# Kernel tuning notes

Measured on AMD Instinct MI355X. Metric: run time of the kernel, lower is better.

The kernel has to match this reference:

```python
import jax, jax.numpy as jnp
import numpy as np

B, T, F, H = 8192, 256, 64, 50

def setup_inputs() -> dict:
    key = jax.random.key(0)
    ks = jax.random.split(key, 6)
    s = 0.1
    x = jax.random.normal(ks[0], (B, T, F), dtype=jnp.float32)
    W = jax.random.normal(ks[1], (F, 3 * H), dtype=jnp.float32) * s   # input kernel [z|r|h]
    U = jax.random.normal(ks[2], (H, 3 * H), dtype=jnp.float32) * s   # recurrent kernel
    b = jax.random.normal(ks[3], (2, 3 * H), dtype=jnp.float32) * s   # [input bias; recurrent bias] (reset_after=True)
    Wd = jax.random.normal(ks[4], (H, 1), dtype=jnp.float32) * s
    bd = jax.random.normal(ks[5], (1,), dtype=jnp.float32) * s
    return {"x": x, "W": W, "U": U, "b": b, "Wd": Wd, "bd": bd}

def _gru_last_hidden(x, W, U, b):
    # Precompute input projections for all timesteps: [B,T,3H]
    xp = jnp.einsum('btf,fg->btg', x, W) + b[0]
    xp = jnp.transpose(xp, (1, 0, 2))  # [T,B,3H] for scan over time
    bi = b[1]

    def step(h, xt):
        rp = h @ U + bi                       # recurrent projection [B,3H]
        xz, xr, xh = jnp.split(xt, 3, axis=-1)
        rz, rr, rh = jnp.split(rp, 3, axis=-1)
        z = jax.nn.sigmoid(xz + rz)
        r = jax.nn.sigmoid(xr + rr)
        hh = jnp.tanh(xh + r * rh)            # reset_after=True formulation
        h_new = z * h + (1.0 - z) * hh
        return h_new, None

    h0 = jnp.zeros((x.shape[0], U.shape[0]), dtype=x.dtype)
    h_last, _ = jax.lax.scan(step, h0, xp)
    return h_last

def reference(x, W, U, b, Wd, bd):
    h = _gru_last_hidden(x, W, U, b)   # [B,H]
    # Dropout is identity at inference time
    return h @ Wd + bd                 # [B,1]
```

## Files before the change

### kernel.cpp

```cpp
#include <hip/hip_runtime.h>
#include <hip/hip_bf16.h>


typedef __attribute__((ext_vector_type(8))) short s16x8;
typedef __attribute__((ext_vector_type(4))) float f32x4;

#define TS 256

__device__ __forceinline__ unsigned short f2bf(float f) {
  unsigned int v = __builtin_bit_cast(unsigned int, f);
  v += 0x7FFFu + ((v >> 16) & 1u);
  return (unsigned short)(v >> 16);
}
__device__ __forceinline__ unsigned int cvtpk(float a, float b) {
  unsigned int r;
  asm("v_cvt_pk_bf16_f32 %0, %1, %2" : "=v"(r) : "v"(a), "v"(b));
  return r;
}
__device__ __forceinline__ float rcpf(float a) {
  return __builtin_amdgcn_rcpf(a);
}

#define RAWBAR()                                                \
  do {                                                          \
    asm volatile("s_waitcnt lgkmcnt(0)" ::: "memory");          \
    __builtin_amdgcn_sched_barrier(0);                          \
    __builtin_amdgcn_s_barrier();                               \
  } while (0)

__global__ __launch_bounds__(256, 2) void gru_fused(
    const float* __restrict__ x,  const float* __restrict__ W,
    const float* __restrict__ U,  const float* __restrict__ b,
    const float* __restrict__ Wd, const float* __restrict__ bdp,
    float* __restrict__ out)
{
  __shared__ __align__(16) unsigned short xbuf[2][2][512];
  __shared__ __align__(16) unsigned short hbuf[2][2][512];
  __shared__ float red[4][16];

  const int tid = threadIdx.x;
  const int l   = tid & 63;
  const int w   = tid >> 6;
  const int lhi = l >> 4, llo = l & 15;
  const int row0 = blockIdx.x << 4;
  const int u = (w << 4) + llo;

  ((unsigned long long*)hbuf)[tid] = 0ULL;

  const float sZR = -1.44269504088896f;
  const float sH  =  2.88539008177793f;
  float bzS = 0.f, brS = 0.f, bh0S = 0.f, bh1S = 0.f;
  if (u < 50) {
    bzS  = sZR * (b[u]      + b[150 + u]);
    brS  = sZR * (b[50 + u] + b[200 + u]);
    bh0S = sH * b[100 + u];
    bh1S = sH * b[250 + u];
  }

  s16x8 breg[3][4];
  #pragma unroll
  for (int g = 0; g < 3; ++g) {
    const float sc = (g < 2) ? sZR : sH;
    #pragma unroll
    for (int kc = 0; kc < 4; ++kc) {
      s16x8 f;
      #pragma unroll
      for (int i = 0; i < 8; ++i) {
        const int k = kc * 32 + lhi * 8 + i;
        float v = 0.f;
        if (u < 50 && k < 114)
          v = (k < 64) ? W[k * 150 + g * 50 + u]
                       : U[(k - 64) * 150 + g * 50 + u];
        f[i] = (short)f2bf(v * sc);
      }
      breg[g][kc] = f;
    }
  }

  const int sc    = tid >> 7;
  const int sla   = (tid >> 1) & 63;
  const int shalf = tid & 1;
  const float* xp = x + (long)(row0 + (sla & 15)) * (TS * 64)
                      + sc * 32 + (sla >> 4) * 8 + shalf * 4;
  unsigned long long* const xd0 =
      (unsigned long long*)&xbuf[0][sc][sla * 8 + shalf * 4];
  unsigned long long* const xd1 =
      (unsigned long long*)&xbuf[1][sc][sla * 8 + shalf * 4];

  unsigned short* const hst =
      &hbuf[0][u >> 5][(((u & 31) >> 3) * 16 + lhi * 4) * 8 + (u & 7)];

  {
    const f32x4 t0 = *(const f32x4*)xp;
    *xd0 = ((unsigned long long)cvtpk(t0[2], t0[3]) << 32) | cvtpk(t0[0], t0[1]);
    const f32x4 t1 = *(const f32x4*)(xp + 64);
    *xd1 = ((unsigned long long)cvtpk(t1[2], t1[3]) << 32) | cvtpk(t1[0], t1[1]);
  }
  f32x4 X0, X1, X2, X3, X4, X5, X6, X7;
  X2 = *(const f32x4*)(xp + 2 * 64);
  X3 = *(const f32x4*)(xp + 3 * 64);
  X4 = *(const f32x4*)(xp + 4 * 64);
  X5 = *(const f32x4*)(xp + 5 * 64);
  __syncthreads();

  f32x4 LA0 = {bzS, bzS, bzS, bzS}, LA1 = {brS, brS, brS, brS},
        LA2 = {bh0S, bh0S, bh0S, bh0S}, LB0, LB1, LB2;
  {
    const s16x8 a0 = *(const s16x8*)&xbuf[0][0][l * 8];
    const s16x8 a1 = *(const s16x8*)&xbuf[0][1][l * 8];
    LA0 = __builtin_amdgcn_mfma_f32_16x16x32_bf16(a0, breg[0][0], LA0, 0,0,0);
    LA0 = __builtin_amdgcn_mfma_f32_16x16x32_bf16(a1, breg[0][1], LA0, 0,0,0);
    LA1 = __builtin_amdgcn_mfma_f32_16x16x32_bf16(a0, breg[1][0], LA1, 0,0,0);
    LA1 = __builtin_amdgcn_mfma_f32_16x16x32_bf16(a1, breg[1][1], LA1, 0,0,0);
    LA2 = __builtin_amdgcn_mfma_f32_16x16x32_bf16(a0, breg[2][0], LA2, 0,0,0);
    LA2 = __builtin_amdgcn_mfma_f32_16x16x32_bf16(a1, breg[2][1], LA2, 0,0,0);
  }
  __syncthreads();

  float h0 = 0.f, h1 = 0.f, h2 = 0.f, h3 = 0.f;

#define STEP(T, XC, XL, C0, C1, C2, N0, N1, N2)                                \
  {                                                                            \
    const int tl = ((T) + 6 > TS - 1) ? (TS - 1) : ((T) + 6);                  \
    XL = *(const f32x4*)(xp + (long)tl * 64);                                  \
    const int PAR = (T) & 1;                                                   \
    const s16x8 a2 = *(const s16x8*)&hbuf[PAR][0][l * 8];                      \
    const s16x8 a3 = *(const s16x8*)&hbuf[PAR][1][l * 8];                      \
    f32x4 g0 = {0.f, 0.f, 0.f, 0.f}, g1 = {0.f, 0.f, 0.f, 0.f};               \
    f32x4 g2 = {bh1S, bh1S, bh1S, bh1S};                                       \
    g0 = __builtin_amdgcn_mfma_f32_16x16x32_bf16(a2, breg[0][2], g0, 0,0,0);   \
    g0 = __builtin_amdgcn_mfma_f32_16x16x32_bf16(a3, breg[0][3], g0, 0,0,0);   \
    g1 = __builtin_amdgcn_mfma_f32_16x16x32_bf16(a2, breg[1][2], g1, 0,0,0);   \
    g1 = __builtin_amdgcn_mfma_f32_16x16x32_bf16(a3, breg[1][3], g1, 0,0,0);   \
    g2 = __builtin_amdgcn_mfma_f32_16x16x32_bf16(a2, breg[2][2], g2, 0,0,0);   \
    g2 = __builtin_amdgcn_mfma_f32_16x16x32_bf16(a3, breg[2][3], g2, 0,0,0);   \
    const s16x8 a0 = *(const s16x8*)&xbuf[PAR ^ 1][0][l * 8];                  \
    const s16x8 a1 = *(const s16x8*)&xbuf[PAR ^ 1][1][l * 8];                  \
    N0 = (f32x4){bzS, bzS, bzS, bzS};                                          \
    N1 = (f32x4){brS, brS, brS, brS};                                          \
    N2 = (f32x4){bh0S, bh0S, bh0S, bh0S};                                      \
    N0 = __builtin_amdgcn_mfma_f32_16x16x32_bf16(a0, breg[0][0], N0, 0,0,0);   \
    N0 = __builtin_amdgcn_mfma_f32_16x16x32_bf16(a1, breg[0][1], N0, 0,0,0);   \
    N1 = __builtin_amdgcn_mfma_f32_16x16x32_bf16(a0, breg[1][0], N1, 0,0,0);   \
    N1 = __builtin_amdgcn_mfma_f32_16x16x32_bf16(a1, breg[1][1], N1, 0,0,0);   \
    N2 = __builtin_amdgcn_mfma_f32_16x16x32_bf16(a0, breg[2][0], N2, 0,0,0);   \
    N2 = __builtin_amdgcn_mfma_f32_16x16x32_bf16(a1, breg[2][1], N2, 0,0,0);   \
    *(PAR ? xd1 : xd0) =                                                       \
        ((unsigned long long)cvtpk(XC[2], XC[3]) << 32) | cvtpk(XC[0], XC[1]); \
    _Pragma("unroll")                                                          \
    for (int r = 0; r < 4; ++r) {                                              \
      float hv = (r == 0) ? h0 : (r == 1) ? h1 : (r == 2) ? h2 : h3;           \
      const float z  = rcpf(1.f + exp2f(C0[r] + g0[r]));                       \
      const float rr = rcpf(1.f + exp2f(C1[r] + g1[r]));                       \
      const float q  = rcpf(1.f + exp2f(fmaf(rr, g2[r], C2[r])));              \
      const float hh = fmaf(-2.f, q, 1.f);                                     \
      hv = fmaf(z, hv - hh, hh);                                               \
      if (r == 0) h0 = hv; else if (r == 1) h1 = hv;                           \
      else if (r == 2) h2 = hv; else h3 = hv;                                  \
      hst[(PAR ^ 1) * 1024 + r * 8] = (unsigned short)cvtpk(hv, 0.f);          \
    }                                                                          \
    RAWBAR();                                                                  \
  }

  for (int t = 0; t < TS; t += 8) {
    STEP(t + 0, X2, X6, LA0, LA1, LA2, LB0, LB1, LB2)
    STEP(t + 1, X3, X7, LB0, LB1, LB2, LA0, LA1, LA2)
    STEP(t + 2, X4, X0, LA0, LA1, LA2, LB0, LB1, LB2)
    STEP(t + 3, X5, X1, LB0, LB1, LB2, LA0, LA1, LA2)
    STEP(t + 4, X6, X2, LA0, LA1, LA2, LB0, LB1, LB2)
    STEP(t + 5, X7, X3, LB0, LB1, LB2, LA0, LA1, LA2)
    STEP(t + 6, X0, X4, LA0, LA1, LA2, LB0, LB1, LB2)
    STEP(t + 7, X1, X5, LB0, LB1, LB2, LA0, LA1, LA2)
  }
#undef STEP

  const float Wdv = (u < 50) ? Wd[u] : 0.f;
  float p0 = h0 * Wdv, p1 = h1 * Wdv, p2 = h2 * Wdv, p3 = h3 * Wdv;
  #pragma unroll
  for (int m = 1; m < 16; m <<= 1) {
    p0 += __shfl_xor(p0, m);
    p1 += __shfl_xor(p1, m);
    p2 += __shfl_xor(p2, m);
    p3 += __shfl_xor(p3, m);
  }
  if (llo == 0) {
    red[w][lhi * 4 + 0] = p0;
    red[w][lhi * 4 + 1] = p1;
    red[w][lhi * 4 + 2] = p2;
    red[w][lhi * 4 + 3] = p3;
  }
  __syncthreads();
  if (tid < 16)
    out[row0 + tid] =
        red[0][tid] + red[1][tid] + red[2][tid] + red[3][tid] + bdp[0];
}

extern "C" void kernel_launch(void* const* d_in, const int* in_sizes, int n_in,
                              void* d_out, int out_size, void* d_ws, size_t ws_size,
                              hipStream_t stream) {
  const float* x   = (const float*)d_in[0];
  const float* W   = (const float*)d_in[1];
  const float* U   = (const float*)d_in[2];
  const float* b   = (const float*)d_in[3];
  const float* Wd  = (const float*)d_in[4];
  const float* bdp = (const float*)d_in[5];
  float* out = (float*)d_out;
  gru_fused<<<dim3(512), dim3(256), 0, stream>>>(x, W, U, b, Wd, bdp, out);
}
```

Measured before the change: 798.1 us.

## Halve rows per block, double grid and occupancy, simplify x pipeline

Each block now handles 8 batch rows instead of 16, and the grid doubles to 1024 blocks. Launch bounds rise to 4 blocks per SM so more independent recurrences can interleave and hide the serial per-step latency. The input projection is no longer software-pipelined one step ahead. It is computed inside the same step, alongside the recurrent MFMAs, with a shallower register prefetch of x. Half of each 16-row MFMA tile is now wasted on zero padding, and only lanes holding real rows run the gate math. That doubles the total MFMA work.

Result: slower. 887.2 us (+11.2%).

```diff
diff --git a/kernel.cpp b/kernel.cpp
--- a/kernel.cpp
+++ b/kernel.cpp
@@ -1,8 +1,8 @@
 #include <hip/hip_runtime.h>
-#include <hip/hip_bf16.h>
 
 
 typedef __attribute__((ext_vector_type(8))) short s16x8;
+typedef __attribute__((ext_vector_type(2))) float f32x2;
 typedef __attribute__((ext_vector_type(4))) float f32x4;
 
 #define TS 256
@@ -28,7 +28,7 @@
     __builtin_amdgcn_s_barrier();                               \
   } while (0)
 
-__global__ __launch_bounds__(256, 2) void gru_fused(
+__global__ __launch_bounds__(256, 4) void gru_fused(
     const float* __restrict__ x,  const float* __restrict__ W,
     const float* __restrict__ U,  const float* __restrict__ b,
     const float* __restrict__ Wd, const float* __restrict__ bdp,
@@ -36,16 +36,19 @@
 {
   __shared__ __align__(16) unsigned short xbuf[2][2][512];
   __shared__ __align__(16) unsigned short hbuf[2][2][512];
-  __shared__ float red[4][16];
+  __shared__ float red[4][8];
 
   const int tid = threadIdx.x;
   const int l   = tid & 63;
   const int w   = tid >> 6;
   const int lhi = l >> 4, llo = l & 15;
-  const int row0 = blockIdx.x << 4;
+  const int row0 = blockIdx.x << 3;
   const int u = (w << 4) + llo;
 
-  ((unsigned long long*)hbuf)[tid] = 0ULL;
+  ((unsigned long long*)xbuf)[tid]       = 0ULL;
+  ((unsigned long long*)xbuf)[tid + 256] = 0ULL;
+  ((unsigned long long*)hbuf)[tid]       = 0ULL;
+  ((unsigned long long*)hbuf)[tid + 256] = 0ULL;
 
   const float sZR = -1.44269504088896f;
   const float sH  =  2.88539008177793f;
@@ -60,7 +63,7 @@
   s16x8 breg[3][4];
   #pragma unroll
   for (int g = 0; g < 3; ++g) {
-    const float sc = (g < 2) ? sZR : sH;
+    const float scg = (g < 2) ? sZR : sH;
     #pragma unroll
     for (int kc = 0; kc < 4; ++kc) {
       s16x8 f;
@@ -71,106 +74,86 @@
         if (u < 50 && k < 114)
           v = (k < 64) ? W[k * 150 + g * 50 + u]
                        : U[(k - 64) * 150 + g * 50 + u];
-        f[i] = (short)f2bf(v * sc);
+        f[i] = (short)f2bf(v * scg);
       }
       breg[g][kc] = f;
     }
   }
 
-  const int sc    = tid >> 7;
-  const int sla   = (tid >> 1) & 63;
-  const int shalf = tid & 1;
-  const float* xp = x + (long)(row0 + (sla & 15)) * (TS * 64)
-                      + sc * 32 + (sla >> 4) * 8 + shalf * 4;
-  unsigned long long* const xd0 =
-      (unsigned long long*)&xbuf[0][sc][sla * 8 + shalf * 4];
-  unsigned long long* const xd1 =
-      (unsigned long long*)&xbuf[1][sc][sla * 8 + shalf * 4];
+  const int sc   = tid >> 7;
+  const int rem  = tid & 127;
+  const int srow = rem >> 4;
+  const int koff = (rem & 15) << 1;
+  const float* xp = x + (long)(row0 + srow) * (TS * 64) + sc * 32 + koff;
+  const int sidx = ((((koff >> 3) * 16 + srow) << 3) + (koff & 7)) >> 1;
+  unsigned int* const xd0 = (unsigned int*)&xbuf[0][sc][0] + sidx;
+  unsigned int* const xd1 = (unsigned int*)&xbuf[1][sc][0] + sidx;
 
   unsigned short* const hst =
-      &hbuf[0][u >> 5][(((u & 31) >> 3) * 16 + lhi * 4) * 8 + (u & 7)];
+      &hbuf[0][u >> 5][((((u & 31) >> 3) * 16 + lhi * 4) << 3) + (u & 7)];
 
   {
-    const f32x4 t0 = *(const f32x4*)xp;
-    *xd0 = ((unsigned long long)cvtpk(t0[2], t0[3]) << 32) | cvtpk(t0[0], t0[1]);
-    const f32x4 t1 = *(const f32x4*)(xp + 64);
-    *xd1 = ((unsigned long long)cvtpk(t1[2], t1[3]) << 32) | cvtpk(t1[0], t1[1]);
+    const f32x2 t0 = *(const f32x2*)xp;
+    *xd0 = cvtpk(t0[0], t0[1]);
   }
-  f32x4 X0, X1, X2, X3, X4, X5, X6, X7;
-  X2 = *(const f32x4*)(xp + 2 * 64);
-  X3 = *(const f32x4*)(xp + 3 * 64);
-  X4 = *(const f32x4*)(xp + 4 * 64);
-  X5 = *(const f32x4*)(xp + 5 * 64);
-  __syncthreads();
-
-  f32x4 LA0 = {bzS, bzS, bzS, bzS}, LA1 = {brS, brS, brS, brS},
-        LA2 = {bh0S, bh0S, bh0S, bh0S}, LB0, LB1, LB2;
-  {
-    const s16x8 a0 = *(const s16x8*)&xbuf[0][0][l * 8];
-    const s16x8 a1 = *(const s16x8*)&xbuf[0][1][l * 8];
-    LA0 = __builtin_amdgcn_mfma_f32_16x16x32_bf16(a0, breg[0][0], LA0, 0,0,0);
-    LA0 = __builtin_amdgcn_mfma_f32_16x16x32_bf16(a1, breg[0][1], LA0, 0,0,0);
-    LA1 = __builtin_amdgcn_mfma_f32_16x16x32_bf16(a0, breg[1][0], LA1, 0,0,0);
-    LA1 = __builtin_amdgcn_mfma_f32_16x16x32_bf16(a1, breg[1][1], LA1, 0,0,0);
-    LA2 = __builtin_amdgcn_mfma_f32_16x16x32_bf16(a0, breg[2][0], LA2, 0,0,0);
-    LA2 = __builtin_amdgcn_mfma_f32_16x16x32_bf16(a1, breg[2][1], LA2, 0,0,0);
-  }
+  f32x2 R0 = *(const f32x2*)(xp + 1 * 64);
+  f32x2 R1 = *(const f32x2*)(xp + 2 * 64);
+  f32x2 R2 = *(const f32x2*)(xp + 3 * 64);
+  f32x2 R3 = *(const f32x2*)(xp + 4 * 64);
   __syncthreads();
 
   float h0 = 0.f, h1 = 0.f, h2 = 0.f, h3 = 0.f;
 
-#define STEP(T, XC, XL, C0, C1, C2, N0, N1, N2)                                \
+#define STEP(T, CUR)                                                           \
   {                                                                            \
-    const int tl = ((T) + 6 > TS - 1) ? (TS - 1) : ((T) + 6);                  \
-    XL = *(const f32x4*)(xp + (long)tl * 64);                                  \
     const int PAR = (T) & 1;                                                   \
+    const s16x8 a0 = *(const s16x8*)&xbuf[PAR][0][l * 8];                      \
+    const s16x8 a1 = *(const s16x8*)&xbuf[PAR][1][l * 8];                      \
     const s16x8 a2 = *(const s16x8*)&hbuf[PAR][0][l * 8];                      \
     const s16x8 a3 = *(const s16x8*)&hbuf[PAR][1][l * 8];                      \
-    f32x4 g0 = {0.f, 0.f, 0.f, 0.f}, g1 = {0.f, 0.f, 0.f, 0.f};               \
-    f32x4 g2 = {bh1S, bh1S, bh1S, bh1S};                                       \
+    f32x4 g0 = {bzS, bzS, bzS, bzS};                                           \
+    g0 = __builtin_amdgcn_mfma_f32_16x16x32_bf16(a0, breg[0][0], g0, 0,0,0);   \
+    g0 = __builtin_amdgcn_mfma_f32_16x16x32_bf16(a1, breg[0][1], g0, 0,0,0);   \
     g0 = __builtin_amdgcn_mfma_f32_16x16x32_bf16(a2, breg[0][2], g0, 0,0,0);   \
     g0 = __builtin_amdgcn_mfma_f32_16x16x32_bf16(a3, breg[0][3], g0, 0,0,0);   \
+    f32x4 g1 = {brS, brS, brS, brS};                                           \
+    g1 = __builtin_amdgcn_mfma_f32_16x16x32_bf16(a0, breg[1][0], g1, 0,0,0);   \
+    g1 = __builtin_amdgcn_mfma_f32_16x16x32_bf16(a1, breg[1][1], g1, 0,0,0);   \
     g1 = __builtin_amdgcn_mfma_f32_16x16x32_bf16(a2, breg[1][2], g1, 0,0,0);   \
     g1 = __builtin_amdgcn_mfma_f32_16x16x32_bf16(a3, breg[1][3], g1, 0,0,0);   \
-    g2 = __builtin_amdgcn_mfma_f32_16x16x32_bf16(a2, breg[2][2], g2, 0,0,0);   \
-    g2 = __builtin_amdgcn_mfma_f32_16x16x32_bf16(a3, breg[2][3], g2, 0,0,0);   \
-    const s16x8 a0 = *(const s16x8*)&xbuf[PAR ^ 1][0][l * 8];                  \
-    const s16x8 a1 = *(const s16x8*)&xbuf[PAR ^ 1][1][l * 8];                  \
-    N0 = (f32x4){bzS, bzS, bzS, bzS};                                          \
-    N1 = (f32x4){brS, brS, brS, brS};                                          \
-    N2 = (f32x4){bh0S, bh0S, bh0S, bh0S};                                      \
-    N0 = __builtin_amdgcn_mfma_f32_16x16x32_bf16(a0, breg[0][0], N0, 0,0,0);   \
-    N0 = __builtin_amdgcn_mfma_f32_16x16x32_bf16(a1, breg[0][1], N0, 0,0,0);   \
-    N1 = __builtin_amdgcn_mfma_f32_16x16x32_bf16(a0, breg[1][0], N1, 0,0,0);   \
-    N1 = __builtin_amdgcn_mfma_f32_16x16x32_bf16(a1, breg[1][1], N1, 0,0,0);   \
-    N2 = __builtin_amdgcn_mfma_f32_16x16x32_bf16(a0, breg[2][0], N2, 0,0,0);   \
-    N2 = __builtin_amdgcn_mfma_f32_16x16x32_bf16(a1, breg[2][1], N2, 0,0,0);   \
-    *(PAR ? xd1 : xd0) =                                                       \
-        ((unsigned long long)cvtpk(XC[2], XC[3]) << 32) | cvtpk(XC[0], XC[1]); \
-    _Pragma("unroll")                                                          \
-    for (int r = 0; r < 4; ++r) {                                              \
-      float hv = (r == 0) ? h0 : (r == 1) ? h1 : (r == 2) ? h2 : h3;           \
-      const float z  = rcpf(1.f + exp2f(C0[r] + g0[r]));                       \
-      const float rr = rcpf(1.f + exp2f(C1[r] + g1[r]));                       \
-      const float q  = rcpf(1.f + exp2f(fmaf(rr, g2[r], C2[r])));              \
-      const float hh = fmaf(-2.f, q, 1.f);                                     \
-      hv = fmaf(z, hv - hh, hh);                                               \
-      if (r == 0) h0 = hv; else if (r == 1) h1 = hv;                           \
-      else if (r == 2) h2 = hv; else h3 = hv;                                  \
-      hst[(PAR ^ 1) * 1024 + r * 8] = (unsigned short)cvtpk(hv, 0.f);          \
+    f32x4 gx = {bh0S, bh0S, bh0S, bh0S};                                       \
+    gx = __builtin_amdgcn_mfma_f32_16x16x32_bf16(a0, breg[2][0], gx, 0,0,0);   \
+    gx = __builtin_amdgcn_mfma_f32_16x16x32_bf16(a1, breg[2][1], gx, 0,0,0);   \
+    f32x4 gh = {bh1S, bh1S, bh1S, bh1S};                                       \
+    gh = __builtin_amdgcn_mfma_f32_16x16x32_bf16(a2, breg[2][2], gh, 0,0,0);   \
+    gh = __builtin_amdgcn_mfma_f32_16x16x32_bf16(a3, breg[2][3], gh, 0,0,0);   \
+    *(PAR ? xd0 : xd1) = cvtpk(CUR[0], CUR[1]);                                \
+    {                                                                          \
+      const int tl = ((T) + 5 > TS - 1) ? (TS - 1) : ((T) + 5);                \
+      CUR = *(const f32x2*)(xp + (long)tl * 64);                               \
+    }                                                                          \
+    if (lhi < 2) {                                                             \
+      _Pragma("unroll")                                                        \
+      for (int r = 0; r < 4; ++r) {                                            \
+        float hv = (r == 0) ? h0 : (r == 1) ? h1 : (r == 2) ? h2 : h3;         \
+        const float z  = rcpf(1.f + exp2f(g0[r]));                             \
+        const float rr = rcpf(1.f + exp2f(g1[r]));                             \
+        const float q  = rcpf(1.f + exp2f(fmaf(rr, gh[r], gx[r])));            \
+        const float hh = fmaf(-2.f, q, 1.f);                                   \
+        hv = fmaf(z, hv - hh, hh);                                             \
+        if (r == 0) h0 = hv; else if (r == 1) h1 = hv;                         \
+        else if (r == 2) h2 = hv; else h3 = hv;                                \
+        hst[((PAR) ^ 1) * 1024 + r * 8] = (unsigned short)cvtpk(hv, 0.f);      \
+      }                                                                        \
     }                                                                          \
     RAWBAR();                                                                  \
   }
 
-  for (int t = 0; t < TS; t += 8) {
-    STEP(t + 0, X2, X6, LA0, LA1, LA2, LB0, LB1, LB2)
-    STEP(t + 1, X3, X7, LB0, LB1, LB2, LA0, LA1, LA2)
-    STEP(t + 2, X4, X0, LA0, LA1, LA2, LB0, LB1, LB2)
-    STEP(t + 3, X5, X1, LB0, LB1, LB2, LA0, LA1, LA2)
-    STEP(t + 4, X6, X2, LA0, LA1, LA2, LB0, LB1, LB2)
-    STEP(t + 5, X7, X3, LB0, LB1, LB2, LA0, LA1, LA2)
-    STEP(t + 6, X0, X4, LA0, LA1, LA2, LB0, LB1, LB2)
-    STEP(t + 7, X1, X5, LB0, LB1, LB2, LA0, LA1, LA2)
+  for (int t = 0; t < TS; t += 4) {
+    STEP(t + 0, R0)
+    STEP(t + 1, R1)
+    STEP(t + 2, R2)
+    STEP(t + 3, R3)
   }
 #undef STEP
 
@@ -183,14 +166,14 @@
     p2 += __shfl_xor(p2, m);
     p3 += __shfl_xor(p3, m);
   }
-  if (llo == 0) {
+  if (llo == 0 && lhi < 2) {
     red[w][lhi * 4 + 0] = p0;
     red[w][lhi * 4 + 1] = p1;
     red[w][lhi * 4 + 2] = p2;
     red[w][lhi * 4 + 3] = p3;
   }
   __syncthreads();
-  if (tid < 16)
+  if (tid < 8)
     out[row0 + tid] =
         red[0][tid] + red[1][tid] + red[2][tid] + red[3][tid] + bdp[0];
 }
@@ -205,5 +188,5 @@
   const float* Wd  = (const float*)d_in[4];
   const float* bdp = (const float*)d_in[5];
   float* out = (float*)d_out;
-  gru_fused<<<dim3(512), dim3(256), 0, stream>>>(x, W, U, b, Wd, bdp, out);
+  gru_fused<<<dim3(1024), dim3(256), 0, stream>>>(x, W, U, b, Wd, bdp, out);
 }
```
